# Kernel tuning notes

Measured on AMD Instinct MI355X. Metric: run time of the kernel, lower is better.

The kernel has to match this reference:

```python
import jax, jax.numpy as jnp
import numpy as np

B, S, H, NH = 2, 2048, 768, 12
HD = H // NH
SCALE = HD ** -0.5


def setup_inputs() -> dict:
    key = jax.random.key(0)
    ks = jax.random.split(key, 12)
    std = H ** -0.5
    return {
        "hidden_states": jax.random.normal(ks[0], (B, S, H), jnp.float32),
        "aspect_weights": jax.random.normal(ks[1], (B, S), jnp.float32),
        "opinion_weights": jax.random.normal(ks[2], (B, S), jnp.float32),
        "attention_mask": jnp.ones((B, S), jnp.int32),
        # stacked params, branch axis order: 0=aspect, 1=opinion, 2=context
        "Wq": jax.random.normal(ks[3], (3, H, H), jnp.float32) * std,
        "bq": jax.random.normal(ks[4], (3, H), jnp.float32) * 0.02,
        "Wk": jax.random.normal(ks[5], (3, H, H), jnp.float32) * std,
        "bk": jax.random.normal(ks[6], (3, H), jnp.float32) * 0.02,
        "Wv": jax.random.normal(ks[7], (3, H, H), jnp.float32) * std,
        "bv": jax.random.normal(ks[8], (3, H), jnp.float32) * 0.02,
        "Wo": jax.random.normal(ks[9], (3, H, H), jnp.float32) * std,
        "bo": jax.random.normal(ks[10], (3, H), jnp.float32) * 0.02,
    }


def _proj(x, W, b):
    # x: [B,S,H], W: [3,H,H], b: [3,H] -> [3,B,nh,S,hd]
    y = jnp.einsum("bsh,nhe->nbse", x, W) + b[:, None, None, :]
    return y.reshape(3, x.shape[0], x.shape[1], NH, HD).transpose(0, 1, 3, 2, 4)


def reference(hidden_states, aspect_weights, opinion_weights, attention_mask,
              Wq, bq, Wk, bk, Wv, bv, Wo, bo):
    q = _proj(hidden_states, Wq, bq)  # [3,B,nh,S,hd]
    k = _proj(hidden_states, Wk, bk)
    v = _proj(hidden_states, Wv, bv)

    mask = (attention_mask == 0)[:, None, None, :]  # [B,1,1,S], True = masked

    def masked_softmax(scores):
        scores = jnp.where(mask, -jnp.inf, scores)
        return jax.nn.softmax(scores, axis=-1)

    scores = jnp.einsum("nbhqd,nbhkd->nbhqk", q, k) * SCALE  # [3,B,nh,S,S]

    a_bias = aspect_weights[:, None, :, None]   # [B,1,S,1] per-query bias
    o_bias = opinion_weights[:, None, :, None]

    p_a = masked_softmax(scores[0] + a_bias)                     # [B,nh,S,S]
    p_o = masked_softmax(scores[1] + o_bias)
    p_c = masked_softmax(scores[2] + 0.5 * (p_a + p_o))

    probs = jnp.stack([p_a, p_o, p_c])                           # [3,B,nh,S,S]
    ctx = jnp.einsum("nbhqk,nbhkd->nbhqd", probs, v)             # [3,B,nh,S,hd]
    ctx = ctx.transpose(0, 1, 3, 2, 4).reshape(3, hidden_states.shape[0], hidden_states.shape[1], H)
    out = jnp.einsum("nbsh,nhe->nbse", ctx, Wo) + bo[:, None, None, :]
    return (out[0], out[1], out[2])
```

## Files before the change

kernel.cpp:

```cpp
#include <hip/hip_runtime.h>
#include <hip/hip_bf16.h>

#define DI __device__ __forceinline__

typedef __bf16 bf16;
typedef bf16  bf16x8 __attribute__((ext_vector_type(8)));
typedef bf16  bf16x4 __attribute__((ext_vector_type(4)));
typedef float f32x4  __attribute__((ext_vector_type(4)));
typedef unsigned int u32x4 __attribute__((ext_vector_type(4)));

static constexpr int Bb = 2, Ss = 2048, Hh = 768, NHh = 12, HDd = 64;
static constexpr float SL2 = 0.125f * 1.4426950408889634f;
static constexpr float C2  = 0.5f   * 1.4426950408889634f;

DI f32x4 zero4() { f32x4 z = {0.f, 0.f, 0.f, 0.f}; return z; }

__global__ __launch_bounds__(256) void conv_x(const float* __restrict__ x,
                                              bf16* __restrict__ xb) {
  int i = blockIdx.x * 256 + threadIdx.x;
  float4 v = ((const float4*)x)[i];
  bf16x4 o;
  o[0] = (bf16)v.x; o[1] = (bf16)v.y; o[2] = (bf16)v.z; o[3] = (bf16)v.w;
  ((bf16x4*)xb)[i] = o;
}

__global__ __launch_bounds__(256) void transpose_w(
    const float* __restrict__ Wq, const float* __restrict__ Wk,
    const float* __restrict__ Wv, const float* __restrict__ Wo,
    bf16* __restrict__ dst) {
  __shared__ float t[32][33];
  const int z = blockIdx.z;
  const int set = z / 3, n = z - set * 3;
  const float* src = (set == 0) ? Wq : (set == 1) ? Wk : (set == 2) ? Wv : Wo;
  src += (size_t)n * Hh * Hh;
  bf16* out = dst + ((size_t)set * 3 + n) * Hh * Hh;
  const int e0 = blockIdx.x * 32, h0 = blockIdx.y * 32;
  const int tx = threadIdx.x, ty = threadIdx.y;
#pragma unroll
  for (int i = 0; i < 4; i++)
    t[ty + 8 * i][tx] = src[(size_t)(h0 + ty + 8 * i) * Hh + e0 + tx];
  __syncthreads();
#pragma unroll
  for (int i = 0; i < 4; i++)
    out[(size_t)(e0 + ty + 8 * i) * Hh + h0 + tx] = (bf16)t[tx][ty + 8 * i];
}

DI void gemm_core128(const bf16* __restrict__ A, const bf16* __restrict__ Bm,
                     int m0, int n0, bf16 (*As)[40], bf16 (*Bs)[40],
                     f32x4 acc[4][4]) {
  const int tid = threadIdx.x;
  const int lane = tid & 63, lg = lane >> 4, lc = lane & 15;
  const int wr = tid >> 7, wc = (tid >> 6) & 1;
  u32x4 ar[2], br[2];
  auto issue = [&](int k0) {
#pragma unroll
    for (int i = 0; i < 2; i++) {
      int c = tid + i * 256, r = c >> 2, o = (c & 3) * 8;
      ar[i] = *(const u32x4*)&A[(size_t)(m0 + r) * Hh + k0 + o];
      br[i] = *(const u32x4*)&Bm[(size_t)(n0 + r) * Hh + k0 + o];
    }
  };
  auto commit = [&]() {
#pragma unroll
    for (int i = 0; i < 2; i++) {
      int c = tid + i * 256, r = c >> 2, o = (c & 3) * 8;
      *(u32x4*)&As[r][o] = ar[i];
      *(u32x4*)&Bs[r][o] = br[i];
    }
  };
  issue(0);
  commit();
  __syncthreads();
  for (int k0 = 0; k0 < Hh; k0 += 32) {
    const bool more = (k0 + 32 < Hh);
    if (more) issue(k0 + 32);
    bf16x8 a[4], b[4];
#pragma unroll
    for (int i = 0; i < 4; i++)
      a[i] = *(const bf16x8*)&As[wr * 64 + i * 16 + lc][lg * 8];
#pragma unroll
    for (int i = 0; i < 4; i++)
      b[i] = *(const bf16x8*)&Bs[wc * 64 + i * 16 + lc][lg * 8];
    __builtin_amdgcn_s_setprio(1);
#pragma unroll
    for (int mi = 0; mi < 4; mi++)
#pragma unroll
      for (int ni = 0; ni < 4; ni++)
        acc[mi][ni] = __builtin_amdgcn_mfma_f32_16x16x32_bf16(
            a[mi], b[ni], acc[mi][ni], 0, 0, 0);
    __builtin_amdgcn_s_setprio(0);
    if (more) {
      __syncthreads();
      commit();
      __syncthreads();
    }
  }
}

__global__ __launch_bounds__(256, 3) void gemm_qkv(
    const bf16* __restrict__ xb, const bf16* __restrict__ Wt,
    const float* __restrict__ bq, const float* __restrict__ bk,
    const float* __restrict__ bv, bf16* __restrict__ qo,
    bf16* __restrict__ ko, bf16* __restrict__ vo) {
  __shared__ bf16 As[128][40], Bs[128][40];
  const int mt = blockIdx.x, nt = blockIdx.y, z = blockIdx.z;
  const int proj = z / 3, n = z - proj * 3;
  const bf16* Wm = Wt + ((size_t)proj * 3 + n) * Hh * Hh;
  const float* bias = ((proj == 0) ? bq : (proj == 1) ? bk : bv) + n * Hh;
  f32x4 acc[4][4];
#pragma unroll
  for (int mi = 0; mi < 4; mi++)
#pragma unroll
    for (int ni = 0; ni < 4; ni++) acc[mi][ni] = zero4();
  gemm_core128(xb, Wm, mt * 128, nt * 128, As, Bs, acc);

  const int tid = threadIdx.x, lane = tid & 63, lg = lane >> 4, lc = lane & 15;
  const int wr = tid >> 7, wc = (tid >> 6) & 1;
  const int rbase = mt * 128 + wr * 64 + lg * 4;
  const int cbase = nt * 128 + wc * 64 + lc;
  if (proj < 2) {
    bf16* out = (proj == 0) ? qo : ko;
#pragma unroll
    for (int ni = 0; ni < 4; ni++) {
      int e = cbase + ni * 16, hi = e >> 6, d = e & 63;
      float bval = bias[e];
#pragma unroll
      for (int mi = 0; mi < 4; mi++) {
        int row = rbase + mi * 16;
        int bidx = row >> 11, ss = row & 2047;
        size_t p = (((size_t)(n * Bb + bidx) * NHh + hi) * Ss + ss) * HDd + d;
#pragma unroll
        for (int r = 0; r < 4; r++)
          out[p + (size_t)r * HDd] = (bf16)(acc[mi][ni][r] + bval);
      }
    }
  } else {
#pragma unroll
    for (int ni = 0; ni < 4; ni++) {
      int e = cbase + ni * 16, hi = e >> 6, d = e & 63;
      float bval = bias[e];
#pragma unroll
      for (int mi = 0; mi < 4; mi++) {
        int row = rbase + mi * 16;
        int bidx = row >> 11, ss = row & 2047;
        bf16x4 pk;
#pragma unroll
        for (int r = 0; r < 4; r++) pk[r] = (bf16)(acc[mi][ni][r] + bval);
        *(bf16x4*)&vo[(((size_t)(n * Bb + bidx) * NHh + hi) * HDd + d) * Ss + ss] = pk;
      }
    }
  }
}

__global__ __launch_bounds__(256, 3) void gemm_out_k(
    const bf16* __restrict__ ctx, const bf16* __restrict__ Wto,
    const float* __restrict__ bo, float* __restrict__ out) {
  __shared__ bf16 As[128][40], Bs[128][40];
  const int mt = blockIdx.x, nt = blockIdx.y;
  const int n = mt >> 5;
  const bf16* Wm = Wto + (size_t)n * Hh * Hh;
  const float* bias = bo + n * Hh;
  f32x4 acc[4][4];
#pragma unroll
  for (int mi = 0; mi < 4; mi++)
#pragma unroll
    for (int ni = 0; ni < 4; ni++) acc[mi][ni] = zero4();
  gemm_core128(ctx, Wm, mt * 128, nt * 128, As, Bs, acc);

  const int tid = threadIdx.x, lane = tid & 63, lg = lane >> 4, lc = lane & 15;
  const int wr = tid >> 7, wc = (tid >> 6) & 1;
  const int rbase = mt * 128 + wr * 64 + lg * 4;
  const int cbase = nt * 128 + wc * 64 + lc;
#pragma unroll
  for (int ni = 0; ni < 4; ni++) {
    int col = cbase + ni * 16;
    float bval = bias[col];
#pragma unroll
    for (int mi = 0; mi < 4; mi++) {
      int row = rbase + mi * 16;
#pragma unroll
      for (int r = 0; r < 4; r++)
        out[(size_t)(row + r) * Hh + col] = acc[mi][ni][r] + bval;
    }
  }
}

__global__ __launch_bounds__(256, 2) void attn_kernel(
    const bf16* __restrict__ q, const bf16* __restrict__ k,
    const bf16* __restrict__ vT, bf16* __restrict__ ctx) {
  __shared__ __align__(16) bf16 smem[24576];

  const int tid = threadIdx.x;
  const int lane = tid & 63, w = tid >> 6;
  const int lg = lane >> 4, lc = lane & 15;
  const int f = blockIdx.x;
  const int j = f >> 3;
  const int bh = (f & 7) * 3 + (j >> 5);
  const int qt = j & 31;
  const int bidx = bh / NHh, hidx = bh - bidx * NHh;
  const int swk = (lc & 7) << 3;

  size_t base[3];
#pragma unroll
  for (int n = 0; n < 3; n++)
    base[n] = ((size_t)(n * Bb + bidx) * NHh + hidx) * (size_t)(Ss * HDd);

  const int qr = qt * 64 + w * 16;

  bf16x8 qf[3][2];
#pragma unroll
  for (int n = 0; n < 3; n++)
#pragma unroll
    for (int sl = 0; sl < 2; sl++)
      qf[n][sl] = *(const bf16x8*)&q[base[n] + (size_t)(qr + lc) * HDd + sl * 32 + lg * 8];

  u32x4 kreg[6], vreg[6];
  auto issueK2 = [&](int kt0) {
#pragma unroll
    for (int i = 0; i < 4; i++) {
      int n_ = i >> 1;
      int rem = (i & 1) * 256 + tid;
      int rr = rem >> 3, o8 = (rem & 7) << 3;
      kreg[i] = *(const u32x4*)&k[base[n_] + (size_t)(kt0 + rr) * HDd + o8];
    }
  };
  auto commitK2 = [&]() {
#pragma unroll
    for (int i = 0; i < 4; i++) {
      int n_ = i >> 1;
      int rem = (i & 1) * 256 + tid;
      int rr = rem >> 3, o8 = (rem & 7) << 3;
      *(u32x4*)&smem[n_ * 4096 + rr * 64 + (o8 ^ ((rr & 7) << 3))] = kreg[i];
    }
  };
  auto issueP2 = [&](int kt0) {
#pragma unroll
    for (int i = 0; i < 6; i++) {
      int n_ = i >> 1;
      int rem = (i & 1) * 256 + tid;
      int rr = rem >> 3, o8 = (rem & 7) << 3;
      kreg[i] = *(const u32x4*)&k[base[n_] + (size_t)(kt0 + rr) * HDd + o8];
      vreg[i] = *(const u32x4*)&vT[base[n_] + (size_t)rr * Ss + kt0 + o8];
    }
  };
  auto commitP2 = [&]() {
#pragma unroll
    for (int i = 0; i < 6; i++) {
      int n_ = i >> 1;
      int rem = (i & 1) * 256 + tid;
      int rr = rem >> 3, o8 = (rem & 7) << 3;
      int sw = o8 ^ ((rr & 7) << 3);
      *(u32x4*)&smem[n_ * 4096 + rr * 64 + sw] = kreg[i];
      *(u32x4*)&smem[12288 + n_ * 4096 + rr * 64 + sw] = vreg[i];
    }
  };

  auto qkt = [&](int n_, f32x4 s[4]) {
    __builtin_amdgcn_s_setprio(1);
#pragma unroll
    for (int t = 0; t < 4; t++) {
      int row = t * 16 + lc;
      bf16x8 a0 = *(const bf16x8*)&smem[n_ * 4096 + row * 64 + ((lg * 8) ^ swk)];
      bf16x8 a1 = *(const bf16x8*)&smem[n_ * 4096 + row * 64 + ((32 + lg * 8) ^ swk)];
      s[t] = __builtin_amdgcn_mfma_f32_16x16x32_bf16(a0, qf[n_][0], s[t], 0, 0, 0);
      s[t] = __builtin_amdgcn_mfma_f32_16x16x32_bf16(a1, qf[n_][1], s[t], 0, 0, 0);
    }
    __builtin_amdgcn_s_setprio(0);
  };

  auto tilestat = [&](const f32x4 s[4], float& m, float& l) {
    float tm = -3.4e38f;
#pragma unroll
    for (int t = 0; t < 4; t++)
#pragma unroll
      for (int r = 0; r < 4; r++) tm = fmaxf(tm, s[t][r]);
    tm *= SL2;
    tm = fmaxf(tm, __shfl_xor(tm, 16));
    tm = fmaxf(tm, __shfl_xor(tm, 32));
    float nm = fmaxf(m, tm);
    float sum = 0.f;
#pragma unroll
    for (int t = 0; t < 4; t++)
#pragma unroll
      for (int r = 0; r < 4; r++)
        sum += __builtin_amdgcn_exp2f(fmaf(s[t][r], SL2, -nm));
    sum += __shfl_xor(sum, 16);
    sum += __shfl_xor(sum, 32);
    l = l * __builtin_amdgcn_exp2f(m - nm) + sum;
    m = nm;
  };

  auto pv = [&](int n_, const bf16x4 pk[4], f32x4 cacc[4]) {
    const bf16* vb = &smem[12288 + n_ * 4096];
    bf16x8 vf0[4], vf1[4];
#pragma unroll
    for (int t = 0; t < 4; t++) {
      int row = t * 16 + lc;
      vf0[t] = *(const bf16x8*)&vb[row * 64 + ((lg * 8) ^ swk)];
      vf1[t] = *(const bf16x8*)&vb[row * 64 + ((32 + lg * 8) ^ swk)];
    }
#pragma unroll
    for (int t = 0; t < 4; t++) {
      int slot = 2 * t + (lg >> 1);
      int swz = ((slot ^ (lc & 7)) << 3) + 4 * (lg & 1);
      *(bf16x4*)&smem[(w * 16 + lc) * 64 + swz] = pk[t];
    }
    asm volatile("s_waitcnt lgkmcnt(0)" ::: "memory");
    __builtin_amdgcn_sched_barrier(0);
    bf16x8 pfa = *(const bf16x8*)&smem[(w * 16 + lc) * 64 + ((lg ^ (lc & 7)) << 3)];
    bf16x8 pfb = *(const bf16x8*)&smem[(w * 16 + lc) * 64 + (((4 + lg) ^ (lc & 7)) << 3)];
    __builtin_amdgcn_s_setprio(1);
#pragma unroll
    for (int t = 0; t < 4; t++) {
      cacc[t] = __builtin_amdgcn_mfma_f32_16x16x32_bf16(pfa, vf0[t], cacc[t], 0, 0, 0);
      cacc[t] = __builtin_amdgcn_mfma_f32_16x16x32_bf16(pfb, vf1[t], cacc[t], 0, 0, 0);
    }
    __builtin_amdgcn_s_setprio(0);
  };

  float m0 = -3.4e38f, l0 = 0.f, m1 = -3.4e38f, l1 = 0.f;
  issueK2(0);
  commitK2();
  __syncthreads();
  for (int kt = 0; kt < Ss; kt += 64) {
    const bool more = (kt + 64 < Ss);
    if (more) issueK2(kt + 64);
    {
      f32x4 s[4] = {zero4(), zero4(), zero4(), zero4()};
      qkt(0, s);
      tilestat(s, m0, l0);
    }
    {
      f32x4 s[4] = {zero4(), zero4(), zero4(), zero4()};
      qkt(1, s);
      tilestat(s, m1, l1);
    }
    if (more) {
      __syncthreads();
      commitK2();
      __syncthreads();
    }
  }
  issueP2(0);
  const float mm0 = m0 + __builtin_amdgcn_logf(l0);
  const float mm1 = m1 + __builtin_amdgcn_logf(l1);

  f32x4 c0[4], c1[4], c2[4];
#pragma unroll
  for (int t = 0; t < 4; t++) { c0[t] = zero4(); c1[t] = zero4(); c2[t] = zero4(); }
  float m2 = -1e30f, l2 = 0.f;

  __syncthreads();
  commitP2();
  __syncthreads();
  for (int kt = 0; kt < Ss; kt += 64) {
    const bool more = (kt + 64 < Ss);
    if (more) issueP2(kt + 64);

    f32x4 pa[4], po[4], p2[4];
    {
      f32x4 s[4] = {zero4(), zero4(), zero4(), zero4()};
      qkt(0, s);
#pragma unroll
      for (int t = 0; t < 4; t++)
#pragma unroll
        for (int r = 0; r < 4; r++)
          pa[t][r] = __builtin_amdgcn_exp2f(fmaf(s[t][r], SL2, -mm0));
    }
    {
      f32x4 s[4] = {zero4(), zero4(), zero4(), zero4()};
      qkt(1, s);
#pragma unroll
      for (int t = 0; t < 4; t++)
#pragma unroll
        for (int r = 0; r < 4; r++)
          po[t][r] = __builtin_amdgcn_exp2f(fmaf(s[t][r], SL2, -mm1));
    }
    {
      f32x4 s[4] = {zero4(), zero4(), zero4(), zero4()};
      qkt(2, s);
#pragma unroll
      for (int t = 0; t < 4; t++)
#pragma unroll
        for (int r = 0; r < 4; r++)
          p2[t][r] = fmaf(s[t][r], SL2, (pa[t][r] + po[t][r]) * C2);
      float tm = -3.4e38f;
#pragma unroll
      for (int t = 0; t < 4; t++)
#pragma unroll
        for (int r = 0; r < 4; r++) tm = fmaxf(tm, p2[t][r]);
      tm = fmaxf(tm, __shfl_xor(tm, 16));
      tm = fmaxf(tm, __shfl_xor(tm, 32));
      if (!__all(tm <= m2 + 8.f)) {
        float nm = fmaxf(m2, tm);
        float al = __builtin_amdgcn_exp2f(m2 - nm);
        float ab[4];
#pragma unroll
        for (int r = 0; r < 4; r++) ab[r] = __shfl(al, 4 * lg + r, 64);
#pragma unroll
        for (int t = 0; t < 4; t++)
#pragma unroll
          for (int r = 0; r < 4; r++) c2[t][r] *= ab[r];
        l2 *= al;
        m2 = nm;
      }
      float sum = 0.f;
#pragma unroll
      for (int t = 0; t < 4; t++)
#pragma unroll
        for (int r = 0; r < 4; r++) {
          p2[t][r] = __builtin_amdgcn_exp2f(p2[t][r] - m2);
          sum += p2[t][r];
        }
      sum += __shfl_xor(sum, 16);
      sum += __shfl_xor(sum, 32);
      l2 += sum;
    }
    bf16x4 pkA[4], pkB[4], pkC[4];
#pragma unroll
    for (int t = 0; t < 4; t++)
#pragma unroll
      for (int r = 0; r < 4; r++) {
        pkA[t][r] = (bf16)pa[t][r];
        pkB[t][r] = (bf16)po[t][r];
        pkC[t][r] = (bf16)p2[t][r];
      }
    __syncthreads();
    pv(0, pkA, c0);
    pv(1, pkB, c1);
    pv(2, pkC, c2);
    if (more) {
      __syncthreads();
      commitP2();
      __syncthreads();
    }
  }

  {
    float il2 = 1.f / l2;
    float ib[4];
#pragma unroll
    for (int r = 0; r < 4; r++) ib[r] = __shfl(il2, 4 * lg + r, 64);
#pragma unroll
    for (int t = 0; t < 4; t++)
#pragma unroll
      for (int r = 0; r < 4; r++) c2[t][r] *= ib[r];
  }
#pragma unroll
  for (int n = 0; n < 3; n++) {
    const f32x4* cc = (n == 0) ? c0 : (n == 1) ? c1 : c2;
#pragma unroll
    for (int t = 0; t < 4; t++)
#pragma unroll
      for (int r = 0; r < 4; r++)
        ctx[((size_t)(n * Bb + bidx) * Ss + qr + 4 * lg + r) * Hh + hidx * HDd +
            t * 16 + lc] = (bf16)cc[t][r];
  }
}

extern "C" void kernel_launch(void* const* d_in, const int* in_sizes, int n_in,
                              void* d_out, int out_size, void* d_ws,
                              size_t ws_size, hipStream_t stream) {
  const float* x  = (const float*)d_in[0];
  const float* Wq = (const float*)d_in[4];
  const float* bq = (const float*)d_in[5];
  const float* Wk = (const float*)d_in[6];
  const float* bk = (const float*)d_in[7];
  const float* Wv = (const float*)d_in[8];
  const float* bv = (const float*)d_in[9];
  const float* Wo = (const float*)d_in[10];
  const float* bo = (const float*)d_in[11];
  float* out = (float*)d_out;

  char* ws = (char*)d_ws;
  bf16* xb  = (bf16*)(ws);
  bf16* Wt  = (bf16*)(ws + 6291456);
  bf16* qb  = (bf16*)(ws + 20447232);
  bf16* kb  = (bf16*)(ws + 39321600);
  bf16* vtb = (bf16*)(ws + 58195968);
  bf16* ctx = (bf16*)(ws + 77070336);

  conv_x<<<3072, 256, 0, stream>>>(x, xb);
  transpose_w<<<dim3(24, 24, 12), dim3(32, 8), 0, stream>>>(Wq, Wk, Wv, Wo, Wt);
  gemm_qkv<<<dim3(32, 6, 9), 256, 0, stream>>>(xb, Wt, bq, bk, bv, qb, kb, vtb);
  attn_kernel<<<768, 256, 0, stream>>>(qb, kb, vtb, ctx);
  gemm_out_k<<<dim3(96, 6), 256, 0, stream>>>(ctx, Wt + (size_t)3 * 3 * 768 * 768,
                                              bo, out);
}
```

Baseline: 414.9 us.

## Build PV A-fragments via lane shuffles instead of LDS round trip, swap MFMA operands

Replaces the per-tile write of bf16 probabilities to shared memory, the following barrier and the read-back with a register-only repack that uses cross-lane shuffles to form the MFMA operand fragments. The PV MFMA operands are swapped (V as A, P as B), so the accumulator is transposed. Each lane now holds one query row, which lets the rescale and final normalisation use the lane's own scalar without broadcast shuffles and allows vectorised bf16x4 context stores. Launch bounds are raised to 3 blocks per CU, which risks register spills. The 16 shuffles per branch also add cross-lane traffic in exchange for removing LDS traffic and a __syncthreads.

```diff
diff --git a/kernel.cpp b/kernel.cpp
--- a/kernel.cpp
+++ b/kernel.cpp
@@ -7,6 +7,7 @@
 typedef bf16  bf16x8 __attribute__((ext_vector_type(8)));
 typedef bf16  bf16x4 __attribute__((ext_vector_type(4)));
 typedef float f32x4  __attribute__((ext_vector_type(4)));
+typedef unsigned int u32;
 typedef unsigned int u32x4 __attribute__((ext_vector_type(4)));
 
 static constexpr int Bb = 2, Ss = 2048, Hh = 768, NHh = 12, HDd = 64;
@@ -185,7 +186,7 @@
   }
 }
 
-__global__ __launch_bounds__(256, 2) void attn_kernel(
+__global__ __launch_bounds__(256, 3) void attn_kernel(
     const bf16* __restrict__ q, const bf16* __restrict__ k,
     const bf16* __restrict__ vT, bf16* __restrict__ ctx) {
   __shared__ __align__(16) bf16 smem[24576];
@@ -290,30 +291,48 @@
     m = nm;
   };
 
-  auto pv = [&](int n_, const bf16x4 pk[4], f32x4 cacc[4]) {
+  auto make_pfrag = [&](const f32x4 p[4], bf16x8& pfa, bf16x8& pfb) {
+    u32 lo[4], hi[4];
+#pragma unroll
+    for (int t = 0; t < 4; t++) {
+      union { bf16x4 v; u32 w[2]; } c;
+      c.v[0] = (bf16)p[t][0]; c.v[1] = (bf16)p[t][1];
+      c.v[2] = (bf16)p[t][2]; c.v[3] = (bf16)p[t][3];
+      lo[t] = c.w[0]; hi[t] = c.w[1];
+    }
+    const int L0 = ((lg & 1) << 5) + lc;
+    const int L1 = L0 + 16;
+    const bool th = (lg & 2) != 0;
+    union { bf16x8 v; u32 w[4]; } fa, fb;
+    {
+      u32 x0 = __shfl((int)lo[0], L0), x1 = __shfl((int)hi[0], L0);
+      u32 x2 = __shfl((int)lo[0], L1), x3 = __shfl((int)hi[0], L1);
+      u32 y0 = __shfl((int)lo[1], L0), y1 = __shfl((int)hi[1], L0);
+      u32 y2 = __shfl((int)lo[1], L1), y3 = __shfl((int)hi[1], L1);
+      fa.w[0] = th ? y0 : x0; fa.w[1] = th ? y1 : x1;
+      fa.w[2] = th ? y2 : x2; fa.w[3] = th ? y3 : x3;
+    }
+    {
+      u32 x0 = __shfl((int)lo[2], L0), x1 = __shfl((int)hi[2], L0);
+      u32 x2 = __shfl((int)lo[2], L1), x3 = __shfl((int)hi[2], L1);
+      u32 y0 = __shfl((int)lo[3], L0), y1 = __shfl((int)hi[3], L0);
+      u32 y2 = __shfl((int)lo[3], L1), y3 = __shfl((int)hi[3], L1);
+      fb.w[0] = th ? y0 : x0; fb.w[1] = th ? y1 : x1;
+      fb.w[2] = th ? y2 : x2; fb.w[3] = th ? y3 : x3;
+    }
+    pfa = fa.v; pfb = fb.v;
+  };
+
+  auto pv = [&](int n_, const bf16x8& pfa, const bf16x8& pfb, f32x4 cacc[4]) {
     const bf16* vb = &smem[12288 + n_ * 4096];
-    bf16x8 vf0[4], vf1[4];
+    __builtin_amdgcn_s_setprio(1);
 #pragma unroll
     for (int t = 0; t < 4; t++) {
       int row = t * 16 + lc;
-      vf0[t] = *(const bf16x8*)&vb[row * 64 + ((lg * 8) ^ swk)];
-      vf1[t] = *(const bf16x8*)&vb[row * 64 + ((32 + lg * 8) ^ swk)];
-    }
-#pragma unroll
-    for (int t = 0; t < 4; t++) {
-      int slot = 2 * t + (lg >> 1);
-      int swz = ((slot ^ (lc & 7)) << 3) + 4 * (lg & 1);
-      *(bf16x4*)&smem[(w * 16 + lc) * 64 + swz] = pk[t];
-    }
-    asm volatile("s_waitcnt lgkmcnt(0)" ::: "memory");
-    __builtin_amdgcn_sched_barrier(0);
-    bf16x8 pfa = *(const bf16x8*)&smem[(w * 16 + lc) * 64 + ((lg ^ (lc & 7)) << 3)];
-    bf16x8 pfb = *(const bf16x8*)&smem[(w * 16 + lc) * 64 + (((4 + lg) ^ (lc & 7)) << 3)];
-    __builtin_amdgcn_s_setprio(1);
-#pragma unroll
-    for (int t = 0; t < 4; t++) {
-      cacc[t] = __builtin_amdgcn_mfma_f32_16x16x32_bf16(pfa, vf0[t], cacc[t], 0, 0, 0);
-      cacc[t] = __builtin_amdgcn_mfma_f32_16x16x32_bf16(pfb, vf1[t], cacc[t], 0, 0, 0);
+      bf16x8 v0 = *(const bf16x8*)&vb[row * 64 + ((lg * 8) ^ swk)];
+      bf16x8 v1 = *(const bf16x8*)&vb[row * 64 + ((32 + lg * 8) ^ swk)];
+      cacc[t] = __builtin_amdgcn_mfma_f32_16x16x32_bf16(v0, pfa, cacc[t], 0, 0, 0);
+      cacc[t] = __builtin_amdgcn_mfma_f32_16x16x32_bf16(v1, pfb, cacc[t], 0, 0, 0);
     }
     __builtin_amdgcn_s_setprio(0);
   };
@@ -394,13 +413,10 @@
       if (!__all(tm <= m2 + 8.f)) {
         float nm = fmaxf(m2, tm);
         float al = __builtin_amdgcn_exp2f(m2 - nm);
-        float ab[4];
-#pragma unroll
-        for (int r = 0; r < 4; r++) ab[r] = __shfl(al, 4 * lg + r, 64);
 #pragma unroll
         for (int t = 0; t < 4; t++)
 #pragma unroll
-          for (int r = 0; r < 4; r++) c2[t][r] *= ab[r];
+          for (int r = 0; r < 4; r++) c2[t][r] *= al;
         l2 *= al;
         m2 = nm;
       }
@@ -416,19 +432,13 @@
       sum += __shfl_xor(sum, 32);
       l2 += sum;
     }
-    bf16x4 pkA[4], pkB[4], pkC[4];
-#pragma unroll
-    for (int t = 0; t < 4; t++)
-#pragma unroll
-      for (int r = 0; r < 4; r++) {
-        pkA[t][r] = (bf16)pa[t][r];
-        pkB[t][r] = (bf16)po[t][r];
-        pkC[t][r] = (bf16)p2[t][r];
-      }
-    __syncthreads();
-    pv(0, pkA, c0);
-    pv(1, pkB, c1);
-    pv(2, pkC, c2);
+    bf16x8 fa0, fb0, fa1, fb1, fa2, fb2;
+    make_pfrag(pa, fa0, fb0);
+    make_pfrag(po, fa1, fb1);
+    make_pfrag(p2, fa2, fb2);
+    pv(0, fa0, fb0, c0);
+    pv(1, fa1, fb1, c1);
+    pv(2, fa2, fb2, c2);
     if (more) {
       __syncthreads();
       commitP2();
@@ -438,23 +448,22 @@
 
   {
     float il2 = 1.f / l2;
-    float ib[4];
-#pragma unroll
-    for (int r = 0; r < 4; r++) ib[r] = __shfl(il2, 4 * lg + r, 64);
 #pragma unroll
     for (int t = 0; t < 4; t++)
 #pragma unroll
-      for (int r = 0; r < 4; r++) c2[t][r] *= ib[r];
+      for (int r = 0; r < 4; r++) c2[t][r] *= il2;
   }
 #pragma unroll
   for (int n = 0; n < 3; n++) {
     const f32x4* cc = (n == 0) ? c0 : (n == 1) ? c1 : c2;
 #pragma unroll
-    for (int t = 0; t < 4; t++)
-#pragma unroll
-      for (int r = 0; r < 4; r++)
-        ctx[((size_t)(n * Bb + bidx) * Ss + qr + 4 * lg + r) * Hh + hidx * HDd +
-            t * 16 + lc] = (bf16)cc[t][r];
+    for (int t = 0; t < 4; t++) {
+      bf16x4 o;
+#pragma unroll
+      for (int r = 0; r < 4; r++) o[r] = (bf16)cc[t][r];
+      *(bf16x4*)&ctx[((size_t)(n * Bb + bidx) * Ss + qr + lc) * Hh + hidx * HDd +
+                     t * 16 + 4 * lg] = o;
+    }
   }
 }
 
```

Result: slower. 646.0 us (+55.7%).
